# Kernel optimization log

Measured on AMD Instinct MI355X. Metric: run time of the kernel, lower is better.

## Reference

```python
import jax, jax.numpy as jnp
import numpy as np

B, T, C, H = 8, 4096, 384, 64

def setup_inputs() -> dict:
    key = jax.random.key(0)
    k1, k2, k3, k4 = jax.random.split(key, 4)
    x = jax.random.normal(k1, (B, T, C), dtype=jnp.float32)
    Wq = jax.random.normal(k2, (C, H), dtype=jnp.float32) / np.sqrt(C)
    Wk = jax.random.normal(k3, (C, H), dtype=jnp.float32) / np.sqrt(C)
    Wv = jax.random.normal(k4, (C, H), dtype=jnp.float32) / np.sqrt(C)
    return {"x": x, "Wq": Wq, "Wk": Wk, "Wv": Wv}

def reference(x, Wq, Wk, Wv):
    # single-head causal self-attention (dropout in eval mode = identity)
    T_ = x.shape[1]
    q = jnp.einsum('btc,ch->bth', x, Wq)   # [B,T,H]
    k = jnp.einsum('btc,ch->bth', x, Wk)   # [B,T,H]
    v = jnp.einsum('btc,ch->bth', x, Wv)   # [B,T,H]
    scale = 1.0 / jnp.sqrt(jnp.float32(Wq.shape[1]))
    wei = jnp.einsum('bth,bsh->bts', q, k) * scale        # [B,T,T]
    causal = jnp.tril(jnp.ones((T_, T_), dtype=bool))
    wei = jnp.where(causal, wei, -jnp.inf)
    wei = jax.nn.softmax(wei, axis=-1)
    out = jnp.einsum('bts,bsh->bth', wei, v)              # [B,T,H]
    return out
```

## Files before the change

### kernel.cpp

```cpp
#include <hip/hip_runtime.h>
#include <hip/hip_bf16.h>
#include <cstdint>
#include <cstddef>

#define BATCH 8
#define SEQ   4096
#define CDIM  384
#define HDIM  64
#define NSPL  8

typedef __attribute__((ext_vector_type(8)))  __bf16 bf16x8;
typedef __attribute__((ext_vector_type(4)))  float  f32x4;
typedef __attribute__((ext_vector_type(16))) float  f32x16;
typedef __attribute__((ext_vector_type(4)))  short  short4v;

#if __has_builtin(__builtin_amdgcn_permlane32_swap)
#define HAVE_PERMLANE 1
#else
#define HAVE_PERMLANE 0
#endif

typedef __attribute__((address_space(3))) char lds_char;
typedef const __attribute__((address_space(1))) char gbl_char;

static __device__ __forceinline__ void gl_lds16(const void* g, void* l) {
  __builtin_amdgcn_global_load_lds((gbl_char*)g, (lds_char*)l, 16, 0, 0);
}

static __device__ __forceinline__ short f2bf(float f) {
  union { float f; uint32_t u; } v; v.f = f;
  uint32_t r = v.u + 0x7fffu + ((v.u >> 16) & 1u);
  return (short)(r >> 16);
}

static __device__ __forceinline__ float bf2f(short s) {
  union { uint32_t u; float f; } t;
  t.u = ((uint32_t)(uint16_t)s) << 16;
  return t.f;
}

static __device__ __forceinline__ uint32_t cvtpk(float lo, float hi) {
  uint32_t r;
  asm("v_cvt_pk_bf16_f32 %0, %1, %2" : "=v"(r) : "v"(lo), "v"(hi));
  return r;
}

static __device__ __forceinline__ float fexp2(float x) {
  float r;
  asm("v_exp_f32 %0, %1" : "=v"(r) : "v"(x));
  return r;
}

static __device__ __forceinline__ f32x4 mfma16(bf16x8 a, bf16x8 b, f32x4 c) {
  return __builtin_amdgcn_mfma_f32_16x16x32_bf16(a, b, c, 0, 0, 0);
}

static __device__ __forceinline__ f32x16 mfma32(bf16x8 a, bf16x8 b, f32x16 c) {
  return __builtin_amdgcn_mfma_f32_32x32x16_bf16(a, b, c, 0, 0, 0);
}

static __device__ __forceinline__ f32x4 zero4() {
  f32x4 z = {0.f, 0.f, 0.f, 0.f};
  return z;
}

static __device__ __forceinline__ float xhalf(float x, int hi) {
#if HAVE_PERMLANE
  union { float f; uint32_t u; } a; a.f = x;
  auto r = __builtin_amdgcn_permlane32_swap(a.u, a.u, false, false);
  union { uint32_t u; float f; } o; o.u = hi ? r[0] : r[1];
  return o.f;
#else
  return __shfl_xor(x, 32, 64);
#endif
}

static __device__ __forceinline__ void swap32(uint32_t& a, uint32_t& b, int hi) {
#if HAVE_PERMLANE
  auto r = __builtin_amdgcn_permlane32_swap(a, b, false, false);
  a = r[0]; b = r[1];
#else
  uint32_t sa = (uint32_t)__shfl_xor((int)a, 32, 64);
  uint32_t sb = (uint32_t)__shfl_xor((int)b, 32, 64);
  uint32_t na = hi ? sb : a;
  uint32_t nb = hi ? b : sa;
  a = na; b = nb;
#endif
}

__global__ __launch_bounds__(256) void wpack_kernel(
    const float* __restrict__ Wq, const float* __restrict__ Wk,
    const float* __restrict__ Wv, short* __restrict__ Wt) {
  int idx = blockIdx.x * 256 + threadIdx.x;
  if (idx >= 192 * CDIM) return;
  int n = idx / CDIM;
  int c = idx - n * CDIM;
  int m = n >> 6, h = n & 63;
  const float* W = (m == 0) ? Wq : (m == 1) ? Wk : Wv;
  float s = (m == 0) ? 0.18033688011112042f : 1.0f;
  Wt[idx] = f2bf(W[c * HDIM + h] * s);
}

#define KPAD 136

__global__ __launch_bounds__(256) void qkv_kernel(
    const float* __restrict__ x, const short* __restrict__ Wt,
    short* __restrict__ qb, short* __restrict__ kb, short* __restrict__ vT) {
  __shared__ short xs[2][64][KPAD];
  const int tid = threadIdx.x;
  const int tokbase = blockIdx.x * 64;
  const float4* xg = (const float4*)(x + (size_t)tokbase * CDIM);

  for (int i = tid; i < 2048; i += 256) {
    int r = i >> 5, c4 = i & 31;
    float4 v = xg[r * 96 + c4];
    uint2 st; st.x = cvtpk(v.x, v.y); st.y = cvtpk(v.z, v.w);
    *(uint2*)&xs[0][r][c4 * 4] = st;
  }
  __syncthreads();

  const int wave = tid >> 6;
  const int lane = tid & 63;
  const int l16  = lane & 15;
  const int lq   = lane >> 4;

  f32x4 acc[4][3];
  #pragma unroll
  for (int ai = 0; ai < 4; ++ai)
    #pragma unroll
    for (int j = 0; j < 3; ++j) acc[ai][j] = zero4();

  for (int ch = 0; ch < 3; ++ch) {
    if (ch < 2) {
      const int nb = (ch + 1) & 1;
      for (int i = tid; i < 2048; i += 256) {
        int r = i >> 5, c4 = i & 31;
        float4 v = xg[r * 96 + (ch + 1) * 32 + c4];
        uint2 st; st.x = cvtpk(v.x, v.y); st.y = cvtpk(v.z, v.w);
        *(uint2*)&xs[nb][r][c4 * 4] = st;
      }
    }
    const int cb = ch & 1;
    #pragma unroll
    for (int kk = 0; kk < 4; ++kk) {
      const int k0 = kk * 32;
      bf16x8 a[4];
      #pragma unroll
      for (int ai = 0; ai < 4; ++ai)
        a[ai] = *(const bf16x8*)&xs[cb][ai * 16 + l16][k0 + lq * 8];
      bf16x8 bb[3];
      #pragma unroll
      for (int j = 0; j < 3; ++j) {
        const int nt = wave * 3 + j;
        bb[j] = *(const bf16x8*)&Wt[(size_t)(nt * 16 + l16) * CDIM +
                                    ch * 128 + k0 + lq * 8];
      }
      #pragma unroll
      for (int ai = 0; ai < 4; ++ai)
        #pragma unroll
        for (int j = 0; j < 3; ++j)
          acc[ai][j] = mfma16(a[ai], bb[j], acc[ai][j]);
    }
    __syncthreads();
  }

  const int b     = tokbase >> 12;
  const int tloc0 = tokbase & (SEQ - 1);
  #pragma unroll
  for (int j = 0; j < 3; ++j) {
    const int col = (wave * 3 + j) * 16 + l16;
    const int mat = col >> 6;
    const int h   = col & 63;
    #pragma unroll
    for (int ai = 0; ai < 4; ++ai) {
      const int row0 = ai * 16 + lq * 4;
      if (mat < 2) {
        short* dst = mat ? kb : qb;
        #pragma unroll
        for (int r = 0; r < 4; ++r)
          dst[(size_t)(tokbase + row0 + r) * HDIM + h] = f2bf(acc[ai][j][r]);
      } else {
        union { uint32_t u[2]; short4v s; } sv;
        sv.u[0] = cvtpk(acc[ai][j][0], acc[ai][j][1]);
        sv.u[1] = cvtpk(acc[ai][j][2], acc[ai][j][3]);
        *(short4v*)&vT[(size_t)(b * HDIM + h) * SEQ + (tloc0 + row0)] = sv.s;
      }
    }
  }
}

__global__ __launch_bounds__(512, 2) void attn_kernel(
    const short* __restrict__ qb, const short* __restrict__ kb,
    const short* __restrict__ vT, short* __restrict__ opart,
    float* __restrict__ lw) {
  __shared__ short kvbuf[2][2][4096];

  const int tid  = threadIdx.x;
  const int wave = tid >> 6;
  const int lane = tid & 63;
  const int l31  = lane & 31;
  const int hi   = lane >> 5;
  const int bid  = blockIdx.x;
  const int b    = bid & 7;
  const int idx  = bid >> 3;
  const int qt   = 15 - (idx >> 3);
  const int part = idx & 7;
  const int nkv  = 4 * qt + 4;
  const int base = nkv >> 3;
  const int rem  = nkv & 7;
  const int scnt = base + (part < rem ? 1 : 0);
  const int sbeg = part * base + (part < rem ? part : rem);
  const int q0   = qt << 8;
  const int qw0  = q0 + wave * 32;
  const size_t bT = (size_t)b * SEQ;

  const char* kg = (const char*)(kb + bT * HDIM);
  const char* vg = (const char*)(vT + (size_t)b * HDIM * SEQ);

  const int rsub = lane >> 3;
  const int gcol = ((lane & 7) << 4) ^ (rsub << 4);
  const int krb  = wave * 8;

  f32x16 oacc[2];
  #pragma unroll
  for (int hb = 0; hb < 2; ++hb)
    #pragma unroll
    for (int r = 0; r < 16; ++r) oacc[hb][r] = 0.f;
  float l = 0.f;

  if (scnt > 0) {
    bf16x8 qf[4];
    {
      const short* qrow = qb + (bT + qw0 + l31) * HDIM + hi * 8;
      #pragma unroll
      for (int t = 0; t < 4; ++t)
        qf[t] = *(const bf16x8*)(qrow + 16 * t);
    }
    const int sw = (l31 & 7) << 4;
    int colk[4];
    #pragma unroll
    for (int t = 0; t < 4; ++t) colk[t] = ((t * 32) + hi * 16) ^ sw;
    const int rbase = l31 * 128;

    {
      const int sf = sbeg << 6;
      gl_lds16(kg + (size_t)(sf + krb + rsub) * 128 + gcol,
               (char*)&kvbuf[0][0][0] + krb * 128);
      gl_lds16(vg + (size_t)(krb + rsub) * 8192 + (size_t)sf * 2 + gcol,
               (char*)&kvbuf[0][1][0] + krb * 128);
    }
    __syncthreads();

    int cur = 0;
    for (int it = 0; it < scnt; ++it) {
      const int s0 = (sbeg + it) << 6;
      if (it + 1 < scnt) {
        const int s1 = s0 + 64;
        const int nb = cur ^ 1;
        gl_lds16(kg + (size_t)(s1 + krb + rsub) * 128 + gcol,
                 (char*)&kvbuf[nb][0][0] + krb * 128);
        gl_lds16(vg + (size_t)(krb + rsub) * 8192 + (size_t)s1 * 2 + gcol,
                 (char*)&kvbuf[nb][1][0] + krb * 128);
      }

      if (s0 <= qw0 + 31) {
        const char* bufc = (const char*)kvbuf + cur * 16384;

        f32x16 sacc[2];
        #pragma unroll
        for (int sb = 0; sb < 2; ++sb) {
          #pragma unroll
          for (int r = 0; r < 16; ++r) sacc[sb][r] = 0.f;
          #pragma unroll
          for (int t = 0; t < 4; ++t) {
            bf16x8 kf = *(const bf16x8*)(bufc + sb * 4096 + rbase + colk[t]);
            sacc[sb] = mfma32(kf, qf[t], sacc[sb]);
          }
        }

        if (s0 + 63 > qw0) {
          const int qg = qw0 + l31;
          #pragma unroll
          for (int sb = 0; sb < 2; ++sb)
            #pragma unroll
            for (int r = 0; r < 16; ++r) {
              const int sg = s0 + sb * 32 + (r & 3) + 8 * (r >> 2) + 4 * hi;
              if (sg > qg) sacc[sb][r] = -3e38f;
            }
        }

        float p[2][16];
        #pragma unroll
        for (int sb = 0; sb < 2; ++sb)
          #pragma unroll
          for (int r = 0; r < 16; ++r)
            p[sb][r] = fexp2(sacc[sb][r]);
        float t8[8];
        #pragma unroll
        for (int sb = 0; sb < 2; ++sb)
          #pragma unroll
          for (int g = 0; g < 4; ++g)
            t8[sb * 4 + g] = (p[sb][4 * g] + p[sb][4 * g + 1]) +
                             (p[sb][4 * g + 2] + p[sb][4 * g + 3]);
        l += ((t8[0] + t8[1]) + (t8[2] + t8[3])) +
             ((t8[4] + t8[5]) + (t8[6] + t8[7]));

        uint32_t w[2][4][2];
        #pragma unroll
        for (int sb = 0; sb < 2; ++sb)
          #pragma unroll
          for (int g = 0; g < 4; ++g) {
            w[sb][g][0] = cvtpk(p[sb][4 * g + 0], p[sb][4 * g + 1]);
            w[sb][g][1] = cvtpk(p[sb][4 * g + 2], p[sb][4 * g + 3]);
          }

        bf16x8 pf[4];
        #pragma unroll
        for (int sb = 0; sb < 2; ++sb)
          #pragma unroll
          for (int t = 0; t < 2; ++t) {
            uint32_t a0 = w[sb][2 * t][0], b0 = w[sb][2 * t + 1][0];
            uint32_t a1 = w[sb][2 * t][1], b1 = w[sb][2 * t + 1][1];
            swap32(a0, b0, hi);
            swap32(a1, b1, hi);
            union { uint32_t u[4]; bf16x8 v; } uu;
            uu.u[0] = a0; uu.u[1] = a1; uu.u[2] = b0; uu.u[3] = b1;
            pf[sb * 2 + t] = uu.v;
          }

        __builtin_amdgcn_s_setprio(1);
        #pragma unroll
        for (int hb = 0; hb < 2; ++hb)
          #pragma unroll
          for (int ks = 0; ks < 4; ++ks) {
            bf16x8 vf = *(const bf16x8*)(bufc + 8192 + hb * 4096 + rbase + colk[ks]);
            oacc[hb] = mfma32(vf, pf[ks], oacc[hb]);
          }
        __builtin_amdgcn_s_setprio(0);
      }

      __syncthreads();
      cur ^= 1;
    }
  }

  l += xhalf(l, hi);

  short* obase = opart + (size_t)part * ((size_t)BATCH * SEQ * HDIM);
  const int q = qw0 + l31;
  #pragma unroll
  for (int hb = 0; hb < 2; ++hb)
    #pragma unroll
    for (int g = 0; g < 4; ++g) {
      uint2 st;
      st.x = cvtpk(oacc[hb][4 * g + 0], oacc[hb][4 * g + 1]);
      st.y = cvtpk(oacc[hb][4 * g + 2], oacc[hb][4 * g + 3]);
      *(uint2*)&obase[(bT + q) * HDIM + hb * 32 + 8 * g + 4 * hi] = st;
    }
  if (hi == 0) lw[part * (BATCH * SEQ) + bT + q] = l;
}

__global__ __launch_bounds__(256) void merge_kernel(
    float* __restrict__ out, const short* __restrict__ opart,
    const float* __restrict__ lw) {
  const int g   = blockIdx.x * 256 + threadIdx.x;
  const int row = g >> 4;
  const int c4  = (g & 15) << 2;
  float ls = 0.f;
  #pragma unroll
  for (int i = 0; i < NSPL; ++i) ls += lw[i * (BATCH * SEQ) + row];
  const size_t stride = (size_t)BATCH * SEQ * HDIM;
  const size_t off = (size_t)row * HDIM + c4;
  float a0 = 0.f, a1 = 0.f, a2 = 0.f, a3 = 0.f;
  #pragma unroll
  for (int i = 0; i < NSPL; ++i) {
    short4v s = *(const short4v*)&opart[i * stride + off];
    a0 += bf2f(s[0]);
    a1 += bf2f(s[1]);
    a2 += bf2f(s[2]);
    a3 += bf2f(s[3]);
  }
  const float inv = 1.0f / ls;
  float4 r;
  r.x = a0 * inv; r.y = a1 * inv; r.z = a2 * inv; r.w = a3 * inv;
  *(float4*)&out[off] = r;
}

extern "C" void kernel_launch(void* const* d_in, const int* in_sizes, int n_in,
                              void* d_out, int out_size, void* d_ws, size_t ws_size,
                              hipStream_t stream) {
  (void)in_sizes; (void)n_in; (void)out_size; (void)ws_size;
  const float* x  = (const float*)d_in[0];
  const float* Wq = (const float*)d_in[1];
  const float* Wk = (const float*)d_in[2];
  const float* Wv = (const float*)d_in[3];

  const size_t qkvb = (size_t)BATCH * SEQ * HDIM * sizeof(short);
  const size_t opb  = (size_t)NSPL * BATCH * SEQ * HDIM * sizeof(short);
  const size_t mlb  = (size_t)NSPL * BATCH * SEQ * sizeof(float);
  char* ws = (char*)d_ws;
  short*  qb    = (short*)(ws);
  short*  kb    = (short*)(ws + qkvb);
  short*  vT    = (short*)(ws + 2 * qkvb);
  short*  opart = (short*)(ws + 3 * qkvb);
  float*  lw    = (float*)(ws + 3 * qkvb + opb);
  short*  Wt    = (short*)(ws + 3 * qkvb + opb + mlb);

  wpack_kernel<<<dim3((192 * CDIM + 255) / 256), dim3(256), 0, stream>>>(Wq, Wk, Wv, Wt);
  qkv_kernel<<<dim3(BATCH * SEQ / 64), dim3(256), 0, stream>>>(x, Wt, qb, kb, vT);
  attn_kernel<<<dim3(1024), dim3(512), 0, stream>>>(qb, kb, vT, opart, lw);
  merge_kernel<<<dim3(BATCH * SEQ * HDIM / 4 / 256), dim3(256), 0, stream>>>(
      (float*)d_out, opart, lw);
}
```

Measured before the change: 68.80 us.

## Process 64 query rows per wave to reuse each K/V fragment twice

Doubles the attention query tile from 256 to 512 rows per block, with each wave now handling two 32-row query groups (A and B). Each K and V fragment read from LDS feeds two MFMAs, halving LDS reads per unit of work. The grid drops from 1024 to 512 blocks and the KV split becomes even across the 8 parts. In exchange, registers roughly double for accumulators and the launch-bounds occupancy hint is removed, so occupancy may fall and the fewer, larger blocks may balance worse across CUs.

```diff
diff --git a/kernel.cpp b/kernel.cpp
--- a/kernel.cpp
+++ b/kernel.cpp
@@ -86,6 +86,56 @@
   uint32_t nb = hi ? b : sa;
   a = na; b = nb;
 #endif
+}
+
+static __device__ __forceinline__ void sm_pack(
+    f32x16 (&sacc)[2], bool mk, int qg, int s0, int hi, float& l,
+    bf16x8 (&pf)[4]) {
+  if (mk) {
+    #pragma unroll
+    for (int sb = 0; sb < 2; ++sb)
+      #pragma unroll
+      for (int r = 0; r < 16; ++r) {
+        const int sg = s0 + sb * 32 + (r & 3) + 8 * (r >> 2) + 4 * hi;
+        if (sg > qg) sacc[sb][r] = -3e38f;
+      }
+  }
+  float p[2][16];
+  #pragma unroll
+  for (int sb = 0; sb < 2; ++sb)
+    #pragma unroll
+    for (int r = 0; r < 16; ++r)
+      p[sb][r] = fexp2(sacc[sb][r]);
+  float t8[8];
+  #pragma unroll
+  for (int sb = 0; sb < 2; ++sb)
+    #pragma unroll
+    for (int g = 0; g < 4; ++g)
+      t8[sb * 4 + g] = (p[sb][4 * g] + p[sb][4 * g + 1]) +
+                       (p[sb][4 * g + 2] + p[sb][4 * g + 3]);
+  l += ((t8[0] + t8[1]) + (t8[2] + t8[3])) +
+       ((t8[4] + t8[5]) + (t8[6] + t8[7]));
+
+  uint32_t w[2][4][2];
+  #pragma unroll
+  for (int sb = 0; sb < 2; ++sb)
+    #pragma unroll
+    for (int g = 0; g < 4; ++g) {
+      w[sb][g][0] = cvtpk(p[sb][4 * g + 0], p[sb][4 * g + 1]);
+      w[sb][g][1] = cvtpk(p[sb][4 * g + 2], p[sb][4 * g + 3]);
+    }
+  #pragma unroll
+  for (int sb = 0; sb < 2; ++sb)
+    #pragma unroll
+    for (int t = 0; t < 2; ++t) {
+      uint32_t a0 = w[sb][2 * t][0], b0 = w[sb][2 * t + 1][0];
+      uint32_t a1 = w[sb][2 * t][1], b1 = w[sb][2 * t + 1][1];
+      swap32(a0, b0, hi);
+      swap32(a1, b1, hi);
+      union { uint32_t u[4]; bf16x8 v; } uu;
+      uu.u[0] = a0; uu.u[1] = a1; uu.u[2] = b0; uu.u[3] = b1;
+      pf[sb * 2 + t] = uu.v;
+    }
 }
 
 __global__ __launch_bounds__(256) void wpack_kernel(
@@ -189,7 +239,7 @@
   }
 }
 
-__global__ __launch_bounds__(512, 2) void attn_kernel(
+__global__ __launch_bounds__(512) void attn_kernel(
     const short* __restrict__ qb, const short* __restrict__ kb,
     const short* __restrict__ vT, short* __restrict__ opart,
     float* __restrict__ lw) {
@@ -203,15 +253,13 @@
   const int bid  = blockIdx.x;
   const int b    = bid & 7;
   const int idx  = bid >> 3;
-  const int qt   = 15 - (idx >> 3);
+  const int qt   = 7 - (idx >> 3);
   const int part = idx & 7;
-  const int nkv  = 4 * qt + 4;
-  const int base = nkv >> 3;
-  const int rem  = nkv & 7;
-  const int scnt = base + (part < rem ? 1 : 0);
-  const int sbeg = part * base + (part < rem ? part : rem);
-  const int q0   = qt << 8;
-  const int qw0  = q0 + wave * 32;
+  const int nkv  = 8 * qt + 8;
+  const int scnt = nkv >> 3;
+  const int sbeg = part * scnt;
+  const int q0   = qt << 9;
+  const int qw0  = q0 + wave * 64;
   const size_t bT = (size_t)b * SEQ;
 
   const char* kg = (const char*)(kb + bT * HDIM);
@@ -221,20 +269,23 @@
   const int gcol = ((lane & 7) << 4) ^ (rsub << 4);
   const int krb  = wave * 8;
 
-  f32x16 oacc[2];
+  f32x16 oA[2], oB[2];
   #pragma unroll
   for (int hb = 0; hb < 2; ++hb)
     #pragma unroll
-    for (int r = 0; r < 16; ++r) oacc[hb][r] = 0.f;
-  float l = 0.f;
-
-  if (scnt > 0) {
-    bf16x8 qf[4];
+    for (int r = 0; r < 16; ++r) { oA[hb][r] = 0.f; oB[hb][r] = 0.f; }
+  float lA = 0.f, lB = 0.f;
+
+  {
+    bf16x8 qfA[4], qfB[4];
     {
-      const short* qrow = qb + (bT + qw0 + l31) * HDIM + hi * 8;
+      const short* qrA = qb + (bT + qw0 + l31) * HDIM + hi * 8;
+      const short* qrB = qrA + 32 * HDIM;
       #pragma unroll
-      for (int t = 0; t < 4; ++t)
-        qf[t] = *(const bf16x8*)(qrow + 16 * t);
+      for (int t = 0; t < 4; ++t) {
+        qfA[t] = *(const bf16x8*)(qrA + 16 * t);
+        qfB[t] = *(const bf16x8*)(qrB + 16 * t);
+      }
     }
     const int sw = (l31 & 7) << 4;
     int colk[4];
@@ -263,70 +314,26 @@
                  (char*)&kvbuf[nb][1][0] + krb * 128);
       }
 
-      if (s0 <= qw0 + 31) {
+      if (s0 <= qw0 + 63) {
         const char* bufc = (const char*)kvbuf + cur * 16384;
 
-        f32x16 sacc[2];
+        f32x16 sA[2], sB[2];
         #pragma unroll
         for (int sb = 0; sb < 2; ++sb) {
           #pragma unroll
-          for (int r = 0; r < 16; ++r) sacc[sb][r] = 0.f;
+          for (int r = 0; r < 16; ++r) { sA[sb][r] = 0.f; sB[sb][r] = 0.f; }
           #pragma unroll
           for (int t = 0; t < 4; ++t) {
             bf16x8 kf = *(const bf16x8*)(bufc + sb * 4096 + rbase + colk[t]);
-            sacc[sb] = mfma32(kf, qf[t], sacc[sb]);
+            sA[sb] = mfma32(kf, qfA[t], sA[sb]);
+            sB[sb] = mfma32(kf, qfB[t], sB[sb]);
           }
         }
 
-        if (s0 + 63 > qw0) {
-          const int qg = qw0 + l31;
-          #pragma unroll
-          for (int sb = 0; sb < 2; ++sb)
-            #pragma unroll
-            for (int r = 0; r < 16; ++r) {
-              const int sg = s0 + sb * 32 + (r & 3) + 8 * (r >> 2) + 4 * hi;
-              if (sg > qg) sacc[sb][r] = -3e38f;
-            }
-        }
-
-        float p[2][16];
-        #pragma unroll
-        for (int sb = 0; sb < 2; ++sb)
-          #pragma unroll
-          for (int r = 0; r < 16; ++r)
-            p[sb][r] = fexp2(sacc[sb][r]);
-        float t8[8];
-        #pragma unroll
-        for (int sb = 0; sb < 2; ++sb)
-          #pragma unroll
-          for (int g = 0; g < 4; ++g)
-            t8[sb * 4 + g] = (p[sb][4 * g] + p[sb][4 * g + 1]) +
-                             (p[sb][4 * g + 2] + p[sb][4 * g + 3]);
-        l += ((t8[0] + t8[1]) + (t8[2] + t8[3])) +
-             ((t8[4] + t8[5]) + (t8[6] + t8[7]));
-
-        uint32_t w[2][4][2];
-        #pragma unroll
-        for (int sb = 0; sb < 2; ++sb)
-          #pragma unroll
-          for (int g = 0; g < 4; ++g) {
-            w[sb][g][0] = cvtpk(p[sb][4 * g + 0], p[sb][4 * g + 1]);
-            w[sb][g][1] = cvtpk(p[sb][4 * g + 2], p[sb][4 * g + 3]);
-          }
-
-        bf16x8 pf[4];
-        #pragma unroll
-        for (int sb = 0; sb < 2; ++sb)
-          #pragma unroll
-          for (int t = 0; t < 2; ++t) {
-            uint32_t a0 = w[sb][2 * t][0], b0 = w[sb][2 * t + 1][0];
-            uint32_t a1 = w[sb][2 * t][1], b1 = w[sb][2 * t + 1][1];
-            swap32(a0, b0, hi);
-            swap32(a1, b1, hi);
-            union { uint32_t u[4]; bf16x8 v; } uu;
-            uu.u[0] = a0; uu.u[1] = a1; uu.u[2] = b0; uu.u[3] = b1;
-            pf[sb * 2 + t] = uu.v;
-          }
+        const bool mk = (s0 + 63 > qw0);
+        bf16x8 pfA[4], pfB[4];
+        sm_pack(sA, mk, qw0 + l31, s0, hi, lA, pfA);
+        sm_pack(sB, mk, qw0 + 32 + l31, s0, hi, lB, pfB);
 
         __builtin_amdgcn_s_setprio(1);
         #pragma unroll
@@ -334,7 +341,8 @@
           #pragma unroll
           for (int ks = 0; ks < 4; ++ks) {
             bf16x8 vf = *(const bf16x8*)(bufc + 8192 + hb * 4096 + rbase + colk[ks]);
-            oacc[hb] = mfma32(vf, pf[ks], oacc[hb]);
+            oA[hb] = mfma32(vf, pfA[ks], oA[hb]);
+            oB[hb] = mfma32(vf, pfB[ks], oB[hb]);
           }
         __builtin_amdgcn_s_setprio(0);
       }
@@ -344,20 +352,28 @@
     }
   }
 
-  l += xhalf(l, hi);
+  lA += xhalf(lA, hi);
+  lB += xhalf(lB, hi);
 
   short* obase = opart + (size_t)part * ((size_t)BATCH * SEQ * HDIM);
-  const int q = qw0 + l31;
+  const int qA = qw0 + l31;
   #pragma unroll
   for (int hb = 0; hb < 2; ++hb)
     #pragma unroll
     for (int g = 0; g < 4; ++g) {
-      uint2 st;
-      st.x = cvtpk(oacc[hb][4 * g + 0], oacc[hb][4 * g + 1]);
-      st.y = cvtpk(oacc[hb][4 * g + 2], oacc[hb][4 * g + 3]);
-      *(uint2*)&obase[(bT + q) * HDIM + hb * 32 + 8 * g + 4 * hi] = st;
-    }
-  if (hi == 0) lw[part * (BATCH * SEQ) + bT + q] = l;
+      uint2 stA, stB;
+      stA.x = cvtpk(oA[hb][4 * g + 0], oA[hb][4 * g + 1]);
+      stA.y = cvtpk(oA[hb][4 * g + 2], oA[hb][4 * g + 3]);
+      stB.x = cvtpk(oB[hb][4 * g + 0], oB[hb][4 * g + 1]);
+      stB.y = cvtpk(oB[hb][4 * g + 2], oB[hb][4 * g + 3]);
+      const int h0 = hb * 32 + 8 * g + 4 * hi;
+      *(uint2*)&obase[(bT + qA) * HDIM + h0]      = stA;
+      *(uint2*)&obase[(bT + qA + 32) * HDIM + h0] = stB;
+    }
+  if (hi == 0) {
+    lw[part * (BATCH * SEQ) + bT + qA]      = lA;
+    lw[part * (BATCH * SEQ) + bT + qA + 32] = lB;
+  }
 }
 
 __global__ __launch_bounds__(256) void merge_kernel(
@@ -408,7 +424,7 @@
 
   wpack_kernel<<<dim3((192 * CDIM + 255) / 256), dim3(256), 0, stream>>>(Wq, Wk, Wv, Wt);
   qkv_kernel<<<dim3(BATCH * SEQ / 64), dim3(256), 0, stream>>>(x, Wt, qb, kb, vT);
-  attn_kernel<<<dim3(1024), dim3(512), 0, stream>>>(qb, kb, vT, opart, lw);
+  attn_kernel<<<dim3(512), dim3(512), 0, stream>>>(qb, kb, vT, opart, lw);
   merge_kernel<<<dim3(BATCH * SEQ * HDIM / 4 / 256), dim3(256), 0, stream>>>(
       (float*)d_out, opart, lw);
 }
```

New measurement: 72.67 us. 5.6% more time.
